# Performance work log

Measured on AMD Instinct MI355X. Metric: run time of the kernel, lower is better.

The kernel has to match this reference:

```python
import jax, jax.numpy as jnp
import numpy as np

N = 10000      # nodes
E = 160000     # edges
MUL = 16       # multiplicity of 0e and 1o irreps
NB = 16        # num radial basis
H = 64         # radial MLP hidden
WN = 4 * MUL * MUL  # tensor-product weight_numel (4 CG paths, uvw weights)


def setup_inputs() -> dict:
    key = jax.random.key(0)
    ks = jax.random.split(key, 10)
    node_features = jax.random.normal(ks[0], (N, 4 * MUL), dtype=jnp.float32)  # [N, 16 + 16*3]
    edge_index = jax.random.randint(ks[1], (2, E), 0, N)
    edge_sh = jax.random.normal(ks[2], (E, 4), dtype=jnp.float32)              # 1x0e + 1x1o
    edge_radial_emb = jax.random.uniform(ks[3], (E, NB), dtype=jnp.float32)
    # RadialMLP params
    w1 = jax.random.normal(ks[4], (NB, H), dtype=jnp.float32) / np.sqrt(NB).astype(np.float32)
    b1 = jnp.zeros((H,), jnp.float32)
    w2 = jax.random.normal(ks[5], (H, WN), dtype=jnp.float32) / np.sqrt(H).astype(np.float32)
    b2 = jnp.zeros((WN,), jnp.float32)
    # equivariant Linear params (one [mul,mul] mix per irrep)
    lin_w0 = jax.random.normal(ks[6], (MUL, MUL), dtype=jnp.float32)
    lin_w1 = jax.random.normal(ks[7], (MUL, MUL), dtype=jnp.float32)
    return dict(node_features=node_features, edge_sh=edge_sh, edge_radial_emb=edge_radial_emb,
                w1=w1, b1=b1, w2=w2, b2=b2, lin_w0=lin_w0, lin_w1=lin_w1,
                edge_index=edge_index)


def reference(node_features, edge_sh, edge_radial_emb, w1, b1, w2, b2, lin_w0, lin_w1, edge_index):
    n = node_features.shape[0]
    src, dst = edge_index[0], edge_index[1]
    # radial MLP -> per-edge tensor-product weights, split into the 4 CG paths
    tpw = jax.nn.silu(edge_radial_emb @ w1 + b1) @ w2 + b2        # [E, 4*MUL*MUL]
    W = tpw.reshape(-1, 4, MUL, MUL)
    W00, W01, W10, W11 = W[:, 0], W[:, 1], W[:, 2], W[:, 3]
    # gather source node features, split into scalar (0e) and vector (1o) parts
    xf = node_features[src]
    xs = xf[:, :MUL]                                              # [E, MUL]
    xv = xf[:, MUL:].reshape(-1, MUL, 3)                          # [E, MUL, 3]
    shs = edge_sh[:, 0:1]                                         # [E, 1]
    shv = edge_sh[:, 1:4]                                         # [E, 3]
    alpha = np.float32(1.0 / np.sqrt(2.0 * MUL))  # path norm: 2 paths feed each output irrep
    inv_sqrt3 = np.float32(1.0 / np.sqrt(3.0))    # w3j(1,1,0) contraction constant
    # scalar messages: 0e*0e->0e and 1o*1o->0e
    msg_s = alpha * (jnp.einsum('eu,euv->ev', xs * shs, W00)
                     + inv_sqrt3 * jnp.einsum('eui,ei,euv->ev', xv, shv, W11))
    # vector messages: 0e*1o->1o and 1o*0e->1o
    msg_v = alpha * (jnp.einsum('eu,euv,ei->evi', xs, W01, shv)
                     + jnp.einsum('eui,euv->evi', xv * shs[:, :, None], W10))
    # scatter-sum messages into destination nodes
    agg_s = jax.ops.segment_sum(msg_s, dst, num_segments=n)       # [N, MUL]
    agg_v = jax.ops.segment_sum(msg_v, dst, num_segments=n)       # [N, MUL, 3]
    # equivariant linear (channel mixing per irrep, 1/sqrt(fan_in) norm)
    s = np.float32(1.0 / np.sqrt(MUL))
    ts = (agg_s @ lin_w0) * s
    tv = jnp.einsum('nui,uv->nvi', agg_v, lin_w1) * s
    # NormActivation: x * silu(||x||)/||x||
    eps = np.float32(1e-8)
    ns = jnp.abs(ts)
    act_s = ts * (jax.nn.silu(ns) / (ns + eps))
    nv = jnp.sqrt(jnp.sum(tv * tv, axis=-1))
    act_v = tv * (jax.nn.silu(nv) / (nv + eps))[..., None]
    # identity skip (input irreps == output irreps)
    return node_features + jnp.concatenate([act_s, act_v.reshape(n, MUL * 3)], axis=-1)
```

## Files before the change

### kernel.cpp

```cpp
#include <hip/hip_runtime.h>
#include <hip/hip_bf16.h>
#include <math.h>

#define EPB 64
#define ALPHA 0.17677669529663687f
#define INV_SQRT3 0.57735026918962576f

typedef __attribute__((ext_vector_type(8))) short short8;
typedef __attribute__((ext_vector_type(4))) float f32x4;

__device__ __forceinline__ float silu_f(float x) { return x / (1.0f + __expf(-x)); }

__device__ __forceinline__ unsigned short bf16_rne(float x) {
  unsigned int u = __float_as_uint(x);
  unsigned int r = u + 0x7fffu + ((u >> 16) & 1u);
  return (unsigned short)(r >> 16);
}

__global__ __launch_bounds__(256) void w2t_kernel(const float* __restrict__ w2,
                                                  unsigned short* __restrict__ w2t) {
  __shared__ unsigned short tile[16][260];
  const int t = threadIdx.x;
  const int k0 = (blockIdx.x & 3) * 16;
  const int c0 = (blockIdx.x >> 2) * 256;
  #pragma unroll
  for (int j = 0; j < 16; ++j)
    tile[j][t] = bf16_rne(w2[(size_t)(k0 + j) * 1024 + c0 + t]);
  __syncthreads();
  union { unsigned short s[16]; uint4 q[2]; } pk;
  #pragma unroll
  for (int j = 0; j < 16; ++j) pk.s[j] = tile[j][t];
  uint4* dst = (uint4*)&w2t[(size_t)(c0 + t) * 64 + k0];
  dst[0] = pk.q[0];
  dst[1] = pk.q[1];
}

__global__ __launch_bounds__(256) void count_kernel(const int* __restrict__ eidx,
                                                    int* __restrict__ deg,
                                                    int* __restrict__ rank, int E) {
  const int e = blockIdx.x * 256 + threadIdx.x;
  if (e < E) rank[e] = atomicAdd(&deg[eidx[E + e]], 1);
}

__global__ __launch_bounds__(256) void scan_kernel(const int* __restrict__ deg,
                                                   int* __restrict__ offs, int N) {
  __shared__ int sums[256];
  const int t = threadIdx.x;
  const int ch = (N + 255) >> 8;
  const int lo = t * ch;
  const int hi = min(lo + ch, N);
  int s = 0;
  for (int i = lo; i < hi; ++i) s += deg[i];
  sums[t] = s;
  __syncthreads();
  #pragma unroll
  for (int d = 1; d < 256; d <<= 1) {
    int v = (t >= d) ? sums[t - d] : 0;
    __syncthreads();
    sums[t] += v;
    __syncthreads();
  }
  int run = sums[t] - s;
  for (int i = lo; i < hi; ++i) { offs[i] = run; run += deg[i]; }
  if (lo < N && hi == N) offs[N] = run;
}

__global__ __launch_bounds__(256, 2) void tfn_edge_kernel(
    const float* __restrict__ nf,
    const float* __restrict__ esh,
    const float* __restrict__ emb,
    const float* __restrict__ w1g,
    const float* __restrict__ b1g,
    const unsigned short* __restrict__ w2t,
    const float* __restrict__ b2g,
    const int*   __restrict__ eidx,
    const int*   __restrict__ rank,
    const int*   __restrict__ offs,
    float* __restrict__ msg,
    float* __restrict__ agg,
    int E, int posmode)
{
  __shared__ __align__(16) unsigned short hsm[EPB * 72];
  __shared__ __align__(16) float fsT[16 * 72];
  __shared__ __align__(16) float fbT[16 * 72];
  __shared__ __align__(16) float fxvT[3 * 16 * 72];
  __shared__ __align__(16) float b2s[1024];
  __shared__ __align__(16) float t01[2 * 1088];
  __shared__ __align__(16) float t2s[1088];
  __shared__ __align__(16) float t3s[3 * 1088];
  __shared__ float shs_l[EPB];
  __shared__ float shv_l[EPB * 3];
  __shared__ int   pos_l[EPB];

  const int tid = threadIdx.x;
  const int ebase = blockIdx.x * EPB;

  float* embs = t01;
  float* w1s  = t01 + 1024;

  {
    const int e = tid >> 2, p = tid & 3;
    int eg = ebase + e; if (eg >= E) eg = E - 1;

    float4 em = *(const float4*)&emb[(size_t)eg * 16 + p * 4];
    *(float4*)&embs[e * 16 + p * 4] = em;

    if (p == 0) {
      float4 sh = *(const float4*)&esh[(size_t)eg * 4];
      shs_l[e] = sh.x;
      shv_l[e * 3 + 0] = sh.y; shv_l[e * 3 + 1] = sh.z; shv_l[e * 3 + 2] = sh.w;
      const int dst = eidx[E + eg];
      pos_l[e] = posmode ? (offs[dst] + rank[eg]) : dst;
    }

    const int src = eidx[eg];
    const float* row = nf + (size_t)src * 64;
    const float sv0 = esh[(size_t)eg * 4 + 1];
    const float sv1 = esh[(size_t)eg * 4 + 2];
    const float sv2 = esh[(size_t)eg * 4 + 3];
    #pragma unroll
    for (int uu = 0; uu < 4; ++uu) {
      const int u = p * 4 + uu;
      const float xs = row[u];
      const float x0 = row[16 + u * 3 + 0];
      const float x1 = row[16 + u * 3 + 1];
      const float x2 = row[16 + u * 3 + 2];
      fsT[u * 72 + e] = xs;
      fbT[u * 72 + e] = x0 * sv0 + x1 * sv1 + x2 * sv2;
      fxvT[(0 * 16 + u) * 72 + e] = x0;
      fxvT[(1 * 16 + u) * 72 + e] = x1;
      fxvT[(2 * 16 + u) * 72 + e] = x2;
    }
  }
  {
    const int r = tid >> 4, q = (tid & 15) * 4;
    *(float4*)&w1s[r * 64 + q] = *(const float4*)&w1g[r * 64 + q];
  }
  *(float4*)&b2s[tid * 4] = *(const float4*)&b2g[tid * 4];
  __syncthreads();

  {
    const int e = tid >> 2, p = tid & 3;
    #pragma unroll
    for (int kk = 0; kk < 16; ++kk) {
      const int c = p * 16 + kk;
      float acc = b1g[c];
      #pragma unroll
      for (int j = 0; j < 16; ++j) acc = fmaf(embs[e * 16 + j], w1s[j * 64 + c], acc);
      hsm[e * 72 + c] = bf16_rne(silu_f(acc));
    }
  }
  __syncthreads();

  const int lane = tid & 63;
  const int sec  = tid >> 6;
  const int q = lane >> 4, m = lane & 15;

  union AF { uint4 u4; short8 s8; };
  AF afr[4][2];
  #pragma unroll
  for (int mt = 0; mt < 4; ++mt)
    #pragma unroll
    for (int ks = 0; ks < 2; ++ks)
      afr[mt][ks].u4 = *(const uint4*)&hsm[(mt * 16 + m) * 72 + ks * 32 + q * 8];

  const float* ftab = (sec == 3) ? fbT : fsT;
  const uint4* w2tq = (const uint4*)w2t;

  float acc [4][4];
  float acc3[4][4][3];
  #pragma unroll
  for (int mt = 0; mt < 4; ++mt)
    #pragma unroll
    for (int r = 0; r < 4; ++r) {
      acc[mt][r] = 0.0f;
      acc3[mt][r][0] = 0.0f; acc3[mt][r][1] = 0.0f; acc3[mt][r][2] = 0.0f;
    }

  #pragma unroll 2
  for (int u = 0; u < 16; ++u) {
    const int col = sec * 256 + u * 16 + m;
    union AF b0, b1;
    const uint4* bp = w2tq + (size_t)col * 8 + q;
    b0.u4 = bp[0];
    b1.u4 = bp[4];
    const float b2v = b2s[col];

    #pragma unroll
    for (int mt = 0; mt < 4; ++mt) {
      f32x4 c = {0.0f, 0.0f, 0.0f, 0.0f};
      c = __builtin_amdgcn_mfma_f32_16x16x32_bf16(afr[mt][0].s8, b0.s8, c, 0, 0, 0);
      c = __builtin_amdgcn_mfma_f32_16x16x32_bf16(afr[mt][1].s8, b1.s8, c, 0, 0, 0);

      if (sec == 2) {
        const float4 f0 = *(const float4*)&fxvT[(0 * 16 + u) * 72 + mt * 16 + q * 4];
        const float4 f1 = *(const float4*)&fxvT[(1 * 16 + u) * 72 + mt * 16 + q * 4];
        const float4 f2 = *(const float4*)&fxvT[(2 * 16 + u) * 72 + mt * 16 + q * 4];
        const float ff0[4] = {f0.x, f0.y, f0.z, f0.w};
        const float ff1[4] = {f1.x, f1.y, f1.z, f1.w};
        const float ff2[4] = {f2.x, f2.y, f2.z, f2.w};
        #pragma unroll
        for (int r = 0; r < 4; ++r) {
          const float tp = c[r] + b2v;
          acc3[mt][r][0] = fmaf(ff0[r], tp, acc3[mt][r][0]);
          acc3[mt][r][1] = fmaf(ff1[r], tp, acc3[mt][r][1]);
          acc3[mt][r][2] = fmaf(ff2[r], tp, acc3[mt][r][2]);
        }
      } else {
        const float4 f = *(const float4*)&ftab[u * 72 + mt * 16 + q * 4];
        const float ff[4] = {f.x, f.y, f.z, f.w};
        #pragma unroll
        for (int r = 0; r < 4; ++r)
          acc[mt][r] = fmaf(ff[r], c[r] + b2v, acc[mt][r]);
      }
    }
  }

  #pragma unroll
  for (int mt = 0; mt < 4; ++mt)
    #pragma unroll
    for (int r = 0; r < 4; ++r) {
      const int e = mt * 16 + q * 4 + r;
      if (sec == 0)      t01[e * 17 + m]        = acc[mt][r] * shs_l[e];
      else if (sec == 1) t2s[e * 17 + m]        = acc[mt][r];
      else if (sec == 3) t01[1088 + e * 17 + m] = acc[mt][r];
      else {
        const float s = shs_l[e];
        t3s[0 * 1088 + e * 17 + m] = acc3[mt][r][0] * s;
        t3s[1 * 1088 + e * 17 + m] = acc3[mt][r][1] * s;
        t3s[2 * 1088 + e * 17 + m] = acc3[mt][r][2] * s;
      }
    }
  __syncthreads();

  {
    const int e = tid >> 2, p = tid & 3;
    if (ebase + e < E) {
      if (posmode) {
        float* mrow = msg + (size_t)pos_l[e] * 64;
        if (p == 0) {
          #pragma unroll
          for (int v = 0; v < 16; v += 4) {
            float4 o;
            o.x = ALPHA * (t01[e * 17 + v + 0] + INV_SQRT3 * t01[1088 + e * 17 + v + 0]);
            o.y = ALPHA * (t01[e * 17 + v + 1] + INV_SQRT3 * t01[1088 + e * 17 + v + 1]);
            o.z = ALPHA * (t01[e * 17 + v + 2] + INV_SQRT3 * t01[1088 + e * 17 + v + 2]);
            o.w = ALPHA * (t01[e * 17 + v + 3] + INV_SQRT3 * t01[1088 + e * 17 + v + 3]);
            *(float4*)&mrow[v] = o;
          }
        } else {
          #pragma unroll
          for (int oo = 0; oo < 16; oo += 4) {
            float vals[4];
            #pragma unroll
            for (int k = 0; k < 4; ++k) {
              const int qq = (p - 1) * 16 + oo + k;
              const int v = qq / 3, i = qq - v * 3;
              vals[k] = ALPHA * (t2s[e * 17 + v] * shv_l[e * 3 + i] + t3s[i * 1088 + e * 17 + v]);
            }
            *(float4*)&mrow[16 + (p - 1) * 16 + oo] = make_float4(vals[0], vals[1], vals[2], vals[3]);
          }
        }
      } else {
        const int dst = pos_l[e];
        if (p == 0) {
          #pragma unroll
          for (int v = 0; v < 16; ++v) {
            const float m2 = ALPHA * (t01[e * 17 + v] + INV_SQRT3 * t01[1088 + e * 17 + v]);
            atomicAdd(&agg[(size_t)dst * 64 + v], m2);
          }
        } else {
          #pragma unroll
          for (int oo = 0; oo < 16; ++oo) {
            const int qq = (p - 1) * 16 + oo;
            const int v = qq / 3, i = qq - v * 3;
            const float sh = shv_l[e * 3 + i];
            const float m2 = ALPHA * (t2s[e * 17 + v] * sh + t3s[i * 1088 + e * 17 + v]);
            atomicAdd(&agg[(size_t)dst * 64 + 16 + qq], m2);
          }
        }
      }
    }
  }
}

__global__ __launch_bounds__(256) void tfn_agg_kernel(const float* __restrict__ msg,
                                                      const int* __restrict__ offs,
                                                      float* __restrict__ out, int N) {
  const int n = blockIdx.x * 4 + (threadIdx.x >> 6);
  const int lane = threadIdx.x & 63;
  if (n >= N) return;
  const int s = offs[n], e = offs[n + 1];
  float acc = 0.0f;
  int j = s;
  for (; j + 1 < e; j += 2) {
    acc += msg[(size_t)j * 64 + lane];
    acc += msg[(size_t)(j + 1) * 64 + lane];
  }
  if (j < e) acc += msg[(size_t)j * 64 + lane];
  out[(size_t)n * 64 + lane] = acc;
}

__global__ __launch_bounds__(256) void tfn_node_kernel(
    const float* __restrict__ nf,
    const float* __restrict__ lw0,
    const float* __restrict__ lw1,
    float* __restrict__ out, int N)
{
  __shared__ float w0s[256], w1s[256];
  const int tid = threadIdx.x;
  w0s[tid] = lw0[tid];
  w1s[tid] = lw1[tid];
  __syncthreads();

  const int n = blockIdx.x * 256 + tid;
  if (n >= N) return;

  float* rowp = out + (size_t)n * 64;
  float as[16], av[16][3];
  #pragma unroll
  for (int u = 0; u < 16; ++u) as[u] = rowp[u];
  #pragma unroll
  for (int u = 0; u < 16; ++u) {
    av[u][0] = rowp[16 + u * 3 + 0];
    av[u][1] = rowp[16 + u * 3 + 1];
    av[u][2] = rowp[16 + u * 3 + 2];
  }
  const float* nfr = nf + (size_t)n * 64;
  float res[64];

  #pragma unroll
  for (int v = 0; v < 16; ++v) {
    float acc = 0.0f;
    #pragma unroll
    for (int u = 0; u < 16; ++u) acc = fmaf(as[u], w0s[u * 16 + v], acc);
    const float ts = 0.25f * acc;
    const float ns = fabsf(ts);
    const float g = (ns / (1.0f + __expf(-ns))) / (ns + 1e-8f);
    res[v] = nfr[v] + ts * g;
  }
  #pragma unroll
  for (int v = 0; v < 16; ++v) {
    float a0 = 0.0f, a1 = 0.0f, a2 = 0.0f;
    #pragma unroll
    for (int u = 0; u < 16; ++u) {
      const float w = w1s[u * 16 + v];
      a0 = fmaf(av[u][0], w, a0);
      a1 = fmaf(av[u][1], w, a1);
      a2 = fmaf(av[u][2], w, a2);
    }
    a0 *= 0.25f; a1 *= 0.25f; a2 *= 0.25f;
    const float nv = sqrtf(a0 * a0 + a1 * a1 + a2 * a2);
    const float g = (nv / (1.0f + __expf(-nv))) / (nv + 1e-8f);
    res[16 + v * 3 + 0] = nfr[16 + v * 3 + 0] + a0 * g;
    res[16 + v * 3 + 1] = nfr[16 + v * 3 + 1] + a1 * g;
    res[16 + v * 3 + 2] = nfr[16 + v * 3 + 2] + a2 * g;
  }
  #pragma unroll
  for (int o = 0; o < 64; o += 4) {
    *(float4*)&rowp[o] = make_float4(res[o], res[o + 1], res[o + 2], res[o + 3]);
  }
}

extern "C" void kernel_launch(void* const* d_in, const int* in_sizes, int n_in,
                              void* d_out, int out_size, void* d_ws, size_t ws_size,
                              hipStream_t stream) {
  const float* nf  = (const float*)d_in[0];
  const float* esh = (const float*)d_in[1];
  const float* emb = (const float*)d_in[2];
  const float* w1  = (const float*)d_in[3];
  const float* b1  = (const float*)d_in[4];
  const float* w2  = (const float*)d_in[5];
  const float* b2  = (const float*)d_in[6];
  const float* lw0 = (const float*)d_in[7];
  const float* lw1 = (const float*)d_in[8];
  const int*   eix = (const int*)d_in[9];

  const int N = in_sizes[0] / 64;
  const int E = in_sizes[9] / 2;
  float* out = (float*)d_out;

  char* ws = (char*)d_ws;
  const size_t o_w2t  = 0;
  const size_t o_deg  = 131072;
  const size_t o_offs = o_deg  + (((size_t)N * 4 + 15) & ~(size_t)15);
  const size_t o_rank = o_offs + (((size_t)(N + 1) * 4 + 15) & ~(size_t)15);
  const size_t o_msg  = (o_rank + (size_t)E * 4 + 255) & ~(size_t)255;
  const size_t need   = o_msg + (size_t)E * 256;
  const int posmode = (ws_size >= need) ? 1 : 0;

  unsigned short* w2t = (unsigned short*)(ws + o_w2t);
  int*   deg  = (int*)(ws + o_deg);
  int*   offs = (int*)(ws + o_offs);
  int*   rankp = (int*)(ws + o_rank);
  float* msg  = (float*)(ws + o_msg);

  w2t_kernel<<<dim3(16), dim3(256), 0, stream>>>(w2, w2t);

  const int eblocks = (E + EPB - 1) / EPB;

  if (posmode) {
    hipMemsetAsync(deg, 0, (size_t)N * 4, stream);
    count_kernel<<<dim3((E + 255) / 256), dim3(256), 0, stream>>>(eix, deg, rankp, E);
    scan_kernel<<<dim3(1), dim3(256), 0, stream>>>(deg, offs, N);
    tfn_edge_kernel<<<dim3(eblocks), dim3(256), 0, stream>>>(
        nf, esh, emb, w1, b1, w2t, b2, eix, rankp, offs, msg, out, E, 1);
    tfn_agg_kernel<<<dim3((N + 3) / 4), dim3(256), 0, stream>>>(msg, offs, out, N);
  } else {
    hipMemsetAsync(out, 0, (size_t)out_size * sizeof(float), stream);
    tfn_edge_kernel<<<dim3(eblocks), dim3(256), 0, stream>>>(
        nf, esh, emb, w1, b1, w2t, b2, eix, nullptr, nullptr, nullptr, out, E, 0);
  }

  const int nblocks = (N + 255) / 256;
  tfn_node_kernel<<<dim3(nblocks), dim3(256), 0, stream>>>(nf, lw0, lw1, out, N);
}
```

Baseline: 222.5 us.

## Remap edge kernel warps to row tiles and fuse aggregation with node update

In the edge kernel each wavefront now owns one 16-edge row tile and loops over all four CG path sections. Before, each wavefront owned one section across all four row tiles. Combining the paths happens in registers, so the transposed LDS staging buffers and the final block barrier are removed, and messages are written straight from the MFMA layout. The aggregation kernel is fused with the linear/NormActivation/skip node kernel, which saves a launch and a full round trip of the aggregated tensor through global memory. The cost is that the w2t B-fragments are now reloaded by every wavefront rather than shared per section, and message stores are scalar and strided instead of float4.

```diff
diff --git a/kernel.cpp b/kernel.cpp
--- a/kernel.cpp
+++ b/kernel.cpp
@@ -81,13 +81,12 @@
     int E, int posmode)
 {
   __shared__ __align__(16) unsigned short hsm[EPB * 72];
+  __shared__ __align__(16) float embs[EPB * 17];
+  __shared__ __align__(16) float w1s[16 * 64];
   __shared__ __align__(16) float fsT[16 * 72];
   __shared__ __align__(16) float fbT[16 * 72];
   __shared__ __align__(16) float fxvT[3 * 16 * 72];
   __shared__ __align__(16) float b2s[1024];
-  __shared__ __align__(16) float t01[2 * 1088];
-  __shared__ __align__(16) float t2s[1088];
-  __shared__ __align__(16) float t3s[3 * 1088];
   __shared__ float shs_l[EPB];
   __shared__ float shv_l[EPB * 3];
   __shared__ int   pos_l[EPB];
@@ -95,18 +94,18 @@
   const int tid = threadIdx.x;
   const int ebase = blockIdx.x * EPB;
 
-  float* embs = t01;
-  float* w1s  = t01 + 1024;
-
   {
     const int e = tid >> 2, p = tid & 3;
     int eg = ebase + e; if (eg >= E) eg = E - 1;
 
-    float4 em = *(const float4*)&emb[(size_t)eg * 16 + p * 4];
-    *(float4*)&embs[e * 16 + p * 4] = em;
+    const float4 em = *(const float4*)&emb[(size_t)eg * 16 + p * 4];
+    embs[e * 17 + p * 4 + 0] = em.x;
+    embs[e * 17 + p * 4 + 1] = em.y;
+    embs[e * 17 + p * 4 + 2] = em.z;
+    embs[e * 17 + p * 4 + 3] = em.w;
 
     if (p == 0) {
-      float4 sh = *(const float4*)&esh[(size_t)eg * 4];
+      const float4 sh = *(const float4*)&esh[(size_t)eg * 4];
       shs_l[e] = sh.x;
       shv_l[e * 3 + 0] = sh.y; shv_l[e * 3 + 1] = sh.z; shv_l[e * 3 + 2] = sh.w;
       const int dst = eidx[E + eg];
@@ -133,8 +132,8 @@
     }
   }
   {
-    const int r = tid >> 4, q = (tid & 15) * 4;
-    *(float4*)&w1s[r * 64 + q] = *(const float4*)&w1g[r * 64 + q];
+    const int r = tid >> 4, c4 = (tid & 15) * 4;
+    *(float4*)&w1s[r * 64 + c4] = *(const float4*)&w1g[r * 64 + c4];
   }
   *(float4*)&b2s[tid * 4] = *(const float4*)&b2g[tid * 4];
   __syncthreads();
@@ -146,159 +145,162 @@
       const int c = p * 16 + kk;
       float acc = b1g[c];
       #pragma unroll
-      for (int j = 0; j < 16; ++j) acc = fmaf(embs[e * 16 + j], w1s[j * 64 + c], acc);
+      for (int j = 0; j < 16; ++j) acc = fmaf(embs[e * 17 + j], w1s[j * 64 + c], acc);
       hsm[e * 72 + c] = bf16_rne(silu_f(acc));
     }
   }
   __syncthreads();
 
   const int lane = tid & 63;
-  const int sec  = tid >> 6;
+  const int mt = tid >> 6;
   const int q = lane >> 4, m = lane & 15;
 
   union AF { uint4 u4; short8 s8; };
-  AF afr[4][2];
-  #pragma unroll
-  for (int mt = 0; mt < 4; ++mt)
-    #pragma unroll
-    for (int ks = 0; ks < 2; ++ks)
-      afr[mt][ks].u4 = *(const uint4*)&hsm[(mt * 16 + m) * 72 + ks * 32 + q * 8];
-
-  const float* ftab = (sec == 3) ? fbT : fsT;
+  AF a0, a1;
+  a0.u4 = *(const uint4*)&hsm[(mt * 16 + m) * 72 + q * 8];
+  a1.u4 = *(const uint4*)&hsm[(mt * 16 + m) * 72 + 32 + q * 8];
+
   const uint4* w2tq = (const uint4*)w2t;
 
-  float acc [4][4];
-  float acc3[4][4][3];
-  #pragma unroll
-  for (int mt = 0; mt < 4; ++mt)
-    #pragma unroll
-    for (int r = 0; r < 4; ++r) {
-      acc[mt][r] = 0.0f;
-      acc3[mt][r][0] = 0.0f; acc3[mt][r][1] = 0.0f; acc3[mt][r][2] = 0.0f;
-    }
+  float t0a[4] = {0, 0, 0, 0};
+  float t1a[4] = {0, 0, 0, 0};
+  float t2a[4] = {0, 0, 0, 0};
+  float t3a[4][3] = {};
 
   #pragma unroll 2
   for (int u = 0; u < 16; ++u) {
-    const int col = sec * 256 + u * 16 + m;
-    union AF b0, b1;
-    const uint4* bp = w2tq + (size_t)col * 8 + q;
-    b0.u4 = bp[0];
-    b1.u4 = bp[4];
-    const float b2v = b2s[col];
+    const float4 fs4 = *(const float4*)&fsT[u * 72 + mt * 16 + q * 4];
+    const float4 fb4 = *(const float4*)&fbT[u * 72 + mt * 16 + q * 4];
+    const float4 fx0 = *(const float4*)&fxvT[(0 * 16 + u) * 72 + mt * 16 + q * 4];
+    const float4 fx1 = *(const float4*)&fxvT[(1 * 16 + u) * 72 + mt * 16 + q * 4];
+    const float4 fx2 = *(const float4*)&fxvT[(2 * 16 + u) * 72 + mt * 16 + q * 4];
+    const float fs[4] = {fs4.x, fs4.y, fs4.z, fs4.w};
+    const float fb[4] = {fb4.x, fb4.y, fb4.z, fb4.w};
+    const float f0[4] = {fx0.x, fx0.y, fx0.z, fx0.w};
+    const float f1[4] = {fx1.x, fx1.y, fx1.z, fx1.w};
+    const float f2[4] = {fx2.x, fx2.y, fx2.z, fx2.w};
 
     #pragma unroll
-    for (int mt = 0; mt < 4; ++mt) {
+    for (int sec = 0; sec < 4; ++sec) {
+      const int col = sec * 256 + u * 16 + m;
+      AF b0, b1;
+      const uint4* bp = w2tq + (size_t)col * 8 + q;
+      b0.u4 = bp[0];
+      b1.u4 = bp[4];
+      const float b2v = b2s[col];
+
       f32x4 c = {0.0f, 0.0f, 0.0f, 0.0f};
-      c = __builtin_amdgcn_mfma_f32_16x16x32_bf16(afr[mt][0].s8, b0.s8, c, 0, 0, 0);
-      c = __builtin_amdgcn_mfma_f32_16x16x32_bf16(afr[mt][1].s8, b1.s8, c, 0, 0, 0);
-
-      if (sec == 2) {
-        const float4 f0 = *(const float4*)&fxvT[(0 * 16 + u) * 72 + mt * 16 + q * 4];
-        const float4 f1 = *(const float4*)&fxvT[(1 * 16 + u) * 72 + mt * 16 + q * 4];
-        const float4 f2 = *(const float4*)&fxvT[(2 * 16 + u) * 72 + mt * 16 + q * 4];
-        const float ff0[4] = {f0.x, f0.y, f0.z, f0.w};
-        const float ff1[4] = {f1.x, f1.y, f1.z, f1.w};
-        const float ff2[4] = {f2.x, f2.y, f2.z, f2.w};
+      c = __builtin_amdgcn_mfma_f32_16x16x32_bf16(a0.s8, b0.s8, c, 0, 0, 0);
+      c = __builtin_amdgcn_mfma_f32_16x16x32_bf16(a1.s8, b1.s8, c, 0, 0, 0);
+
+      if (sec == 0) {
+        #pragma unroll
+        for (int r = 0; r < 4; ++r) t0a[r] = fmaf(fs[r], c[r] + b2v, t0a[r]);
+      } else if (sec == 1) {
+        #pragma unroll
+        for (int r = 0; r < 4; ++r) t2a[r] = fmaf(fs[r], c[r] + b2v, t2a[r]);
+      } else if (sec == 2) {
         #pragma unroll
         for (int r = 0; r < 4; ++r) {
           const float tp = c[r] + b2v;
-          acc3[mt][r][0] = fmaf(ff0[r], tp, acc3[mt][r][0]);
-          acc3[mt][r][1] = fmaf(ff1[r], tp, acc3[mt][r][1]);
-          acc3[mt][r][2] = fmaf(ff2[r], tp, acc3[mt][r][2]);
+          t3a[r][0] = fmaf(f0[r], tp, t3a[r][0]);
+          t3a[r][1] = fmaf(f1[r], tp, t3a[r][1]);
+          t3a[r][2] = fmaf(f2[r], tp, t3a[r][2]);
         }
       } else {
-        const float4 f = *(const float4*)&ftab[u * 72 + mt * 16 + q * 4];
-        const float ff[4] = {f.x, f.y, f.z, f.w};
         #pragma unroll
-        for (int r = 0; r < 4; ++r)
-          acc[mt][r] = fmaf(ff[r], c[r] + b2v, acc[mt][r]);
+        for (int r = 0; r < 4; ++r) t1a[r] = fmaf(fb[r], c[r] + b2v, t1a[r]);
       }
     }
   }
 
   #pragma unroll
-  for (int mt = 0; mt < 4; ++mt)
-    #pragma unroll
-    for (int r = 0; r < 4; ++r) {
-      const int e = mt * 16 + q * 4 + r;
-      if (sec == 0)      t01[e * 17 + m]        = acc[mt][r] * shs_l[e];
-      else if (sec == 1) t2s[e * 17 + m]        = acc[mt][r];
-      else if (sec == 3) t01[1088 + e * 17 + m] = acc[mt][r];
-      else {
-        const float s = shs_l[e];
-        t3s[0 * 1088 + e * 17 + m] = acc3[mt][r][0] * s;
-        t3s[1 * 1088 + e * 17 + m] = acc3[mt][r][1] * s;
-        t3s[2 * 1088 + e * 17 + m] = acc3[mt][r][2] * s;
+  for (int r = 0; r < 4; ++r) {
+    const int e_row = mt * 16 + q * 4 + r;
+    if (ebase + e_row < E) {
+      const float shs_e = shs_l[e_row];
+      const float sv0 = shv_l[e_row * 3 + 0];
+      const float sv1 = shv_l[e_row * 3 + 1];
+      const float sv2 = shv_l[e_row * 3 + 2];
+      const float s  = ALPHA * (t0a[r] * shs_e + INV_SQRT3 * t1a[r]);
+      const float v0 = ALPHA * (t2a[r] * sv0 + t3a[r][0] * shs_e);
+      const float v1 = ALPHA * (t2a[r] * sv1 + t3a[r][1] * shs_e);
+      const float v2 = ALPHA * (t2a[r] * sv2 + t3a[r][2] * shs_e);
+      if (posmode) {
+        float* mrow = msg + (size_t)pos_l[e_row] * 64;
+        mrow[m] = s;
+        mrow[16 + m * 3 + 0] = v0;
+        mrow[16 + m * 3 + 1] = v1;
+        mrow[16 + m * 3 + 2] = v2;
+      } else {
+        float* arow = agg + (size_t)pos_l[e_row] * 64;
+        atomicAdd(&arow[m], s);
+        atomicAdd(&arow[16 + m * 3 + 0], v0);
+        atomicAdd(&arow[16 + m * 3 + 1], v1);
+        atomicAdd(&arow[16 + m * 3 + 2], v2);
       }
     }
-  __syncthreads();
-
+  }
+}
+
+__global__ __launch_bounds__(256) void tfn_agg_node_kernel(
+    const float* __restrict__ msg, const int* __restrict__ offs,
+    const float* __restrict__ nf, const float* __restrict__ lw0,
+    const float* __restrict__ lw1, float* __restrict__ out, int N)
+{
+  __shared__ float ag[4 * 68];
+  __shared__ float w0s[256], w1s[256];
+  const int t = threadIdx.x;
+  w0s[t] = lw0[t];
+  w1s[t] = lw1[t];
+
+  const int n0 = blockIdx.x * 4;
   {
-    const int e = tid >> 2, p = tid & 3;
-    if (ebase + e < E) {
-      if (posmode) {
-        float* mrow = msg + (size_t)pos_l[e] * 64;
-        if (p == 0) {
-          #pragma unroll
-          for (int v = 0; v < 16; v += 4) {
-            float4 o;
-            o.x = ALPHA * (t01[e * 17 + v + 0] + INV_SQRT3 * t01[1088 + e * 17 + v + 0]);
-            o.y = ALPHA * (t01[e * 17 + v + 1] + INV_SQRT3 * t01[1088 + e * 17 + v + 1]);
-            o.z = ALPHA * (t01[e * 17 + v + 2] + INV_SQRT3 * t01[1088 + e * 17 + v + 2]);
-            o.w = ALPHA * (t01[e * 17 + v + 3] + INV_SQRT3 * t01[1088 + e * 17 + v + 3]);
-            *(float4*)&mrow[v] = o;
-          }
-        } else {
-          #pragma unroll
-          for (int oo = 0; oo < 16; oo += 4) {
-            float vals[4];
-            #pragma unroll
-            for (int k = 0; k < 4; ++k) {
-              const int qq = (p - 1) * 16 + oo + k;
-              const int v = qq / 3, i = qq - v * 3;
-              vals[k] = ALPHA * (t2s[e * 17 + v] * shv_l[e * 3 + i] + t3s[i * 1088 + e * 17 + v]);
-            }
-            *(float4*)&mrow[16 + (p - 1) * 16 + oo] = make_float4(vals[0], vals[1], vals[2], vals[3]);
-          }
-        }
-      } else {
-        const int dst = pos_l[e];
-        if (p == 0) {
-          #pragma unroll
-          for (int v = 0; v < 16; ++v) {
-            const float m2 = ALPHA * (t01[e * 17 + v] + INV_SQRT3 * t01[1088 + e * 17 + v]);
-            atomicAdd(&agg[(size_t)dst * 64 + v], m2);
-          }
-        } else {
-          #pragma unroll
-          for (int oo = 0; oo < 16; ++oo) {
-            const int qq = (p - 1) * 16 + oo;
-            const int v = qq / 3, i = qq - v * 3;
-            const float sh = shv_l[e * 3 + i];
-            const float m2 = ALPHA * (t2s[e * 17 + v] * sh + t3s[i * 1088 + e * 17 + v]);
-            atomicAdd(&agg[(size_t)dst * 64 + 16 + qq], m2);
-          }
-        }
+    const int w = t >> 6, lane = t & 63;
+    const int n = n0 + w;
+    if (n < N) {
+      const int s = offs[n], e = offs[n + 1];
+      float acc = 0.0f;
+      int j = s;
+      for (; j + 1 < e; j += 2)
+        acc += msg[(size_t)j * 64 + lane] + msg[(size_t)(j + 1) * 64 + lane];
+      if (j < e) acc += msg[(size_t)j * 64 + lane];
+      ag[w * 68 + lane] = acc;
+    }
+  }
+  __syncthreads();
+  {
+    const int node = t >> 6, c = t & 63;
+    const int n = n0 + node;
+    if (n >= N) return;
+    const float* a = &ag[node * 68];
+    float val;
+    if (c < 16) {
+      float accv = 0.0f;
+      #pragma unroll
+      for (int u = 0; u < 16; ++u) accv = fmaf(a[u], w0s[u * 16 + c], accv);
+      const float ts = 0.25f * accv;
+      const float ns = fabsf(ts);
+      const float g = (ns / (1.0f + __expf(-ns))) / (ns + 1e-8f);
+      val = ts * g;
+    } else {
+      const int cc = c - 16;
+      const int v = cc / 3, i = cc - v * 3;
+      float a0 = 0.0f, a1 = 0.0f, a2 = 0.0f;
+      #pragma unroll
+      for (int u = 0; u < 16; ++u) {
+        const float w = w1s[u * 16 + v];
+        a0 = fmaf(a[16 + u * 3 + 0], w, a0);
+        a1 = fmaf(a[16 + u * 3 + 1], w, a1);
+        a2 = fmaf(a[16 + u * 3 + 2], w, a2);
       }
-    }
-  }
-}
-
-__global__ __launch_bounds__(256) void tfn_agg_kernel(const float* __restrict__ msg,
-                                                      const int* __restrict__ offs,
-                                                      float* __restrict__ out, int N) {
-  const int n = blockIdx.x * 4 + (threadIdx.x >> 6);
-  const int lane = threadIdx.x & 63;
-  if (n >= N) return;
-  const int s = offs[n], e = offs[n + 1];
-  float acc = 0.0f;
-  int j = s;
-  for (; j + 1 < e; j += 2) {
-    acc += msg[(size_t)j * 64 + lane];
-    acc += msg[(size_t)(j + 1) * 64 + lane];
-  }
-  if (j < e) acc += msg[(size_t)j * 64 + lane];
-  out[(size_t)n * 64 + lane] = acc;
+      a0 *= 0.25f; a1 *= 0.25f; a2 *= 0.25f;
+      const float nv = sqrtf(a0 * a0 + a1 * a1 + a2 * a2);
+      const float g = (nv / (1.0f + __expf(-nv))) / (nv + 1e-8f);
+      val = ((i == 0) ? a0 : (i == 1) ? a1 : a2) * g;
+    }
+    out[(size_t)n * 64 + c] = nf[(size_t)n * 64 + c] + val;
+  }
 }
 
 __global__ __launch_bounds__(256) void tfn_node_kernel(
@@ -405,13 +407,12 @@
     scan_kernel<<<dim3(1), dim3(256), 0, stream>>>(deg, offs, N);
     tfn_edge_kernel<<<dim3(eblocks), dim3(256), 0, stream>>>(
         nf, esh, emb, w1, b1, w2t, b2, eix, rankp, offs, msg, out, E, 1);
-    tfn_agg_kernel<<<dim3((N + 3) / 4), dim3(256), 0, stream>>>(msg, offs, out, N);
+    tfn_agg_node_kernel<<<dim3((N + 3) / 4), dim3(256), 0, stream>>>(
+        msg, offs, nf, lw0, lw1, out, N);
   } else {
     hipMemsetAsync(out, 0, (size_t)out_size * sizeof(float), stream);
     tfn_edge_kernel<<<dim3(eblocks), dim3(256), 0, stream>>>(
         nf, esh, emb, w1, b1, w2t, b2, eix, nullptr, nullptr, nullptr, out, E, 0);
-  }
-
-  const int nblocks = (N + 255) / 256;
-  tfn_node_kernel<<<dim3(nblocks), dim3(256), 0, stream>>>(nf, lw0, lw1, out, N);
-}
+    tfn_node_kernel<<<dim3((N + 255) / 256), dim3(256), 0, stream>>>(nf, lw0, lw1, out, N);
+  }
+}
```

New measurement: 287.9 us. 29.4% more time.
